# Optimization experiments

Measured on AMD Instinct MI355X. Metric: run time of the kernel, lower is better.

The kernel has to match this reference:

```python
import jax, jax.numpy as jnp
import numpy as np

B = 128      # graphs in batch
NPG = 128    # nodes per graph
F = 256      # num_node_features
D = 192      # d_model
NH = 8       # decoder heads
L = 4        # decoder layers
DFF = 512
DEG = 16     # avg degree
P = 32       # num_patch_nodes
EH = 96      # encoder_hidden = max(D//2, 48)
GH = 4       # GAT heads (layer 1)
EPS = 1e-5


def _init(key, shape, fan_in):
    return jax.random.normal(key, shape, jnp.float32) / np.sqrt(fan_in)


def setup_inputs() -> dict:
    key = jax.random.key(0)
    ks = jax.random.split(key, 40)
    N = B * NPG
    E = N * DEG
    off = jnp.repeat(jnp.arange(B, dtype=jnp.int32) * NPG, E // B)
    src = jax.random.randint(ks[1], (E,), 0, NPG, dtype=jnp.int32) + off
    dst = jax.random.randint(ks[2], (E,), 0, NPG, dtype=jnp.int32) + off
    inp = dict(
        subgraph_x=jax.random.normal(ks[0], (N, F), jnp.float32),
        subgraph_edge_index=jnp.stack([src, dst]),
        target_local_idx=jax.random.randint(ks[3], (B,), 0, NPG, dtype=jnp.int32),
        batch=jnp.repeat(jnp.arange(B, dtype=jnp.int32), NPG),
        num_patch_nodes=P,
    )
    # GAT encoder params (PyG GATConv layout: W [heads*out, in], att [heads, out])
    inp['gat1_w'] = _init(ks[4], (GH * EH, F), F)
    inp['gat1_att_src'] = _init(ks[5], (GH, EH), EH)
    inp['gat1_att_dst'] = _init(ks[6], (GH, EH), EH)
    inp['gat1_b'] = jnp.zeros((GH * EH,), jnp.float32)
    inp['gat2_w'] = _init(ks[7], (D, GH * EH), GH * EH)
    inp['gat2_att_src'] = _init(ks[8], (1, D), D)
    inp['gat2_att_dst'] = _init(ks[9], (1, D), D)
    inp['gat2_b'] = jnp.zeros((D,), jnp.float32)
    # TransformerDecoder layers (stacked over L)
    inp['sa_qkv_w'] = _init(ks[10], (L, 3 * D, D), D)
    inp['sa_qkv_b'] = jnp.zeros((L, 3 * D), jnp.float32)
    inp['sa_out_w'] = _init(ks[11], (L, D, D), D)
    inp['sa_out_b'] = jnp.zeros((L, D), jnp.float32)
    inp['ca_qkv_w'] = _init(ks[12], (L, 3 * D, D), D)
    inp['ca_qkv_b'] = jnp.zeros((L, 3 * D), jnp.float32)
    inp['ca_out_w'] = _init(ks[13], (L, D, D), D)
    inp['ca_out_b'] = jnp.zeros((L, D), jnp.float32)
    inp['ff1_w'] = _init(ks[14], (L, DFF, D), D)
    inp['ff1_b'] = jnp.zeros((L, DFF), jnp.float32)
    inp['ff2_w'] = _init(ks[15], (L, D, DFF), DFF)
    inp['ff2_b'] = jnp.zeros((L, D), jnp.float32)
    inp['ln_g'] = jnp.ones((L, 3, D), jnp.float32)
    inp['ln_b'] = jnp.zeros((L, 3, D), jnp.float32)
    # feature head
    inp['h1_w'] = _init(ks[16], (D, D), D)
    inp['h1_b'] = jnp.zeros((D,), jnp.float32)
    inp['h2_w'] = _init(ks[17], (F, D), D)
    inp['h2_b'] = jnp.zeros((F,), jnp.float32)
    return inp


def _gat(x, src, dst, W, a_src, a_dst, bias, heads, ch, concat):
    # PyG GATConv with add_self_loops=True, negative_slope=0.2, eval mode (no dropout)
    N = x.shape[0]
    xp = (x @ W.T).reshape(N, heads, ch)
    loop = jnp.arange(N, dtype=src.dtype)
    s = jnp.concatenate([src, loop])
    d = jnp.concatenate([dst, loop])
    al_s = (xp * a_src).sum(-1)  # [N, H]
    al_d = (xp * a_dst).sum(-1)
    e = jax.nn.leaky_relu(al_s[s] + al_d[d], 0.2)  # [E+N, H]
    emax = jax.ops.segment_max(e, d, num_segments=N)
    ex = jnp.exp(e - emax[d])
    den = jax.ops.segment_sum(ex, d, num_segments=N)
    coef = ex / (den[d] + 1e-16)
    out = jax.ops.segment_sum(xp[s] * coef[:, :, None], d, num_segments=N)  # [N,H,C]
    out = out.reshape(N, heads * ch) if concat else out.mean(1)
    return out + bias


def _ln(x, g, b):
    m = x.mean(-1, keepdims=True)
    v = ((x - m) ** 2).mean(-1, keepdims=True)
    return (x - m) / jnp.sqrt(v + EPS) * g + b


def _mha(q_in, kv_in, qkv_w, qkv_b, out_w, out_b, causal):
    b, sq, d = q_in.shape
    sk = kv_in.shape[1]
    dh = d // NH
    wq, wk, wv = jnp.split(qkv_w, 3, axis=0)
    bq, bk, bv = jnp.split(qkv_b, 3)
    q = (q_in @ wq.T + bq).reshape(b, sq, NH, dh).transpose(0, 2, 1, 3)
    k = (kv_in @ wk.T + bk).reshape(b, sk, NH, dh).transpose(0, 2, 1, 3)
    v = (kv_in @ wv.T + bv).reshape(b, sk, NH, dh).transpose(0, 2, 1, 3)
    sc = jnp.einsum('bhqd,bhkd->bhqk', q, k) / np.sqrt(dh).astype(np.float32)
    if causal:
        sc = jnp.where(jnp.tril(jnp.ones((sq, sk), bool)), sc, -1e30)
    a = jax.nn.softmax(sc, axis=-1)
    o = jnp.einsum('bhqk,bhkd->bhqd', a, v).transpose(0, 2, 1, 3).reshape(b, sq, d)
    return o @ out_w.T + out_b


def _pe(max_len, d):
    pos = jnp.arange(max_len, dtype=jnp.float32)[:, None]
    div = jnp.exp(jnp.arange(0, d, 2, dtype=jnp.float32) * (-np.log(10000.0) / d))
    pe = jnp.zeros((max_len, d), jnp.float32)
    return pe.at[:, 0::2].set(jnp.sin(pos * div)).at[:, 1::2].set(jnp.cos(pos * div))


def _forward(subgraph_x, gat1_w, gat1_att_src, gat1_att_dst, gat1_b,
             gat2_w, gat2_att_src, gat2_att_dst, gat2_b,
             sa_qkv_w, sa_qkv_b, sa_out_w, sa_out_b,
             ca_qkv_w, ca_qkv_b, ca_out_w, ca_out_b,
             ff1_w, ff1_b, ff2_w, ff2_b, ln_g, ln_b,
             h1_w, h1_b, h2_w, h2_b,
             subgraph_edge_index, target_local_idx, batch, num_patch_nodes):
    src, dst = subgraph_edge_index[0], subgraph_edge_index[1]
    h = jax.nn.elu(_gat(subgraph_x, src, dst, gat1_w, gat1_att_src, gat1_att_dst, gat1_b, GH, EH, True))
    mem = _gat(h, src, dst, gat2_w, gat2_att_src, gat2_att_dst, gat2_b, 1, D, False)
    bsz = target_local_idx.shape[0]
    mem_d = mem.reshape(bsz, -1, D)  # to_dense_batch: equal-sized, sorted graphs -> reshape, mask all-valid
    tgt = mem_d[jnp.arange(bsz), target_local_idx][:, None, :]  # [B,1,D]
    Pn = int(num_patch_nodes)
    pe = _pe(Pn + 1, D)
    feats = []
    adj = jnp.zeros((bsz, Pn + 1, Pn + 1), subgraph_x.dtype)
    for i in range(Pn):
        s = i + 1
        x = tgt + pe[None, :s]  # pos encoding (dropout is eval no-op)
        for l in range(L):
            x = _ln(x + _mha(x, x, sa_qkv_w[l], sa_qkv_b[l], sa_out_w[l], sa_out_b[l], True), ln_g[l, 0], ln_b[l, 0])
            x = _ln(x + _mha(x, mem_d, ca_qkv_w[l], ca_qkv_b[l], ca_out_w[l], ca_out_b[l], False), ln_g[l, 1], ln_b[l, 1])
            ff = jax.nn.gelu(x @ ff1_w[l].T + ff1_b[l], approximate=False) @ ff2_w[l].T + ff2_b[l]
            x = _ln(x + ff, ln_g[l, 2], ln_b[l, 2])
        last = x[:, -1]  # [B,D]
        feats.append(jax.nn.gelu(last @ h1_w.T + h1_b, approximate=False) @ h2_w.T + h2_b)
        cl = jnp.einsum('bsd,bd->bs', x, last)  # connection logits, len s
        adj = adj.at[:, i, Pn].set(cl[:, 0]).at[:, Pn, i].set(cl[:, 0])
        if i > 0:
            adj = adj.at[:, i, :i].set(cl[:, 1:i + 1]).at[:, :i, i].set(cl[:, 1:i + 1])
        tgt = jnp.concatenate([tgt, jax.lax.stop_gradient(last)[:, None]], axis=1)  # .detach() in torch
    adj = jnp.triu(adj, 1)
    adj = adj + jnp.swapaxes(adj, -1, -2)  # symmetric, zero diagonal
    return jnp.stack(feats, axis=1), adj


def reference(subgraph_x, subgraph_edge_index, target_local_idx, batch, num_patch_nodes,
              gat1_w, gat1_att_src, gat1_att_dst, gat1_b,
              gat2_w, gat2_att_src, gat2_att_dst, gat2_b,
              sa_qkv_w, sa_qkv_b, sa_out_w, sa_out_b,
              ca_qkv_w, ca_qkv_b, ca_out_w, ca_out_b,
              ff1_w, ff1_b, ff2_w, ff2_b, ln_g, ln_b,
              h1_w, h1_b, h2_w, h2_b):
    return _forward(subgraph_x, gat1_w, gat1_att_src, gat1_att_dst, gat1_b,
                    gat2_w, gat2_att_src, gat2_att_dst, gat2_b,
                    sa_qkv_w, sa_qkv_b, sa_out_w, sa_out_b,
                    ca_qkv_w, ca_qkv_b, ca_out_w, ca_out_b,
                    ff1_w, ff1_b, ff2_w, ff2_b, ln_g, ln_b,
                    h1_w, h1_b, h2_w, h2_b,
                    subgraph_edge_index, target_local_idx, batch, num_patch_nodes)
```

## Files before the change

kernel.cpp:

```cpp
#include <hip/hip_runtime.h>
#include <hip/hip_bf16.h>
#include <math.h>

#define DEV __device__ __forceinline__
typedef unsigned int u32;
typedef unsigned short u16;

constexpr int NNODES = 16384;
constexpr int NEDGE  = 262144;
constexpr int NEL    = NEDGE + NNODES;
constexpr int FIN    = 256;
constexpr int C1     = 384;
constexpr int DM     = 192;
constexpr int BZ     = 128;
constexpr int NPG_   = 128;
constexpr int LL     = 4;
constexpr int PP     = 32;
constexpr int SM     = 33;
constexpr int DFF_   = 512;

constexpr int PL4     = 52224;
constexpr int OFF4_QKV = 0;
constexpr int OFF4_SAO = 13824;
constexpr int OFF4_CAQ = 18432;
constexpr int OFF4_CAO = 23040;
constexpr int OFF4_FF1 = 27648;
constexpr int OFF4_FF2 = 39936;
constexpr int OFF4_H1  = 4*PL4;
constexpr int OFF4_H2  = OFF4_H1 + 4608;

constexpr size_t O_KVK = 0;
constexpr size_t O_VT  = 6291456;
constexpr size_t O_XP1 = 0;
constexpr size_t O_H   = 6291456;
constexpr size_t O_XP2 = 12582912;
constexpr size_t O_MEM = 15728640;
constexpr size_t O_VSAT= 18874368;
constexpr size_t O_WP  = 20545536;
constexpr size_t O_PE  = 21424128;
constexpr size_t O_AL1S= O_PE + 6336;
constexpr size_t O_AL1D= O_AL1S + 65536;
constexpr size_t O_AL2S= O_AL1D + 65536;
constexpr size_t O_AL2D= O_AL2S + 16384;
constexpr size_t O_CNT = O_AL2D + 16384;
constexpr size_t O_BASE= O_CNT + 16384;
constexpr size_t O_FILL= O_BASE + 16384;
constexpr size_t O_CSRC= O_FILL + 16384;

DEV float gelu_f(float v) { return 0.5f*v*(1.0f + erff(v*0.7071067811865475f)); }
DEV float bflo(u32 w) { return __uint_as_float(w << 16); }
DEV float bfhi(u32 w) { return __uint_as_float(w & 0xffff0000u); }
DEV float bfu(u16 u)  { return __uint_as_float(((u32)u) << 16); }
DEV u16 bf16u(float a) {
  __hip_bfloat16 h = __float2bfloat16(a);
  return *reinterpret_cast<u16*>(&h);
}
DEV u32 pk2(float a, float b) {
  return (u32)bf16u(a) | ((u32)bf16u(b) << 16);
}
DEV void fma8(float& a, uint4 w, float4 xa, float4 xb) {
  a = fmaf(bflo(w.x), xa.x, a); a = fmaf(bfhi(w.x), xa.y, a);
  a = fmaf(bflo(w.y), xa.z, a); a = fmaf(bfhi(w.y), xa.w, a);
  a = fmaf(bflo(w.z), xb.x, a); a = fmaf(bfhi(w.z), xb.y, a);
  a = fmaf(bflo(w.w), xb.z, a); a = fmaf(bfhi(w.w), xb.w, a);
}
template<int NU4, int STRIDE>
DEV float dotcol(const uint4* __restrict__ col, const float* __restrict__ xv) {
  const float4* x4 = (const float4*)xv;
  float a0 = 0, a1 = 0, a2 = 0, a3 = 0;
  #pragma unroll
  for (int q = 0; q < NU4; ++q) {
    uint4 w = col[(size_t)q*STRIDE];
    if ((q & 3) == 0) fma8(a0, w, x4[2*q], x4[2*q+1]);
    else if ((q & 3) == 1) fma8(a1, w, x4[2*q], x4[2*q+1]);
    else if ((q & 3) == 2) fma8(a2, w, x4[2*q], x4[2*q+1]);
    else fma8(a3, w, x4[2*q], x4[2*q+1]);
  }
  return (a0+a1)+(a2+a3);
}

__global__ void zero_kernel(float* adj, int* cnt, int* fill) {
  int i = blockIdx.x*256 + threadIdx.x;
  if (i < BZ*SM*SM) adj[i] = 0.f;
  if (i < NNODES) { cnt[i] = 0; fill[i] = 0; }
}

__global__ void pe_kernel(float* pe) {
  int idx = blockIdx.x*256 + threadIdx.x;
  if (idx >= SM*DM) return;
  int p = idx / DM, d = idx % DM;
  int i2 = d >> 1;
  float div = __expf((float)(2*i2) * (-9.210340371976184f / (float)DM));
  float a = (float)p * div;
  pe[idx] = (d & 1) ? cosf(a) : sinf(a);
}

__global__ void pack_kernel(const float* __restrict__ W, uint4* __restrict__ P, int N, int K) {
  int idx = blockIdx.x*256 + threadIdx.x;
  if (idx >= N*(K>>3)) return;
  int o = idx % N, kq = idx / N;
  const float* r = W + (size_t)o*K + 8*kq;
  uint4 u;
  u.x = pk2(r[0], r[1]); u.y = pk2(r[2], r[3]);
  u.z = pk2(r[4], r[5]); u.w = pk2(r[6], r[7]);
  P[idx] = u;
}

template<int BMODE, bool BF16OUT>
__global__ __launch_bounds__(256) void gemm_nt(const float* __restrict__ A,
    const float* __restrict__ W, const float* __restrict__ bias,
    float* __restrict__ Cf, __hip_bfloat16* __restrict__ Cb, int M, int N, int K)
{
  __shared__ float As[16][68];
  __shared__ float Ws[16][68];
  const int bm = blockIdx.y*64, bn = blockIdx.x*64;
  const int t = threadIdx.x, tx = t & 15, ty = t >> 4;
  float acc[4][4] = {};
  for (int k0 = 0; k0 < K; k0 += 16) {
    #pragma unroll
    for (int i = 0; i < 4; ++i) {
      int idx = t + i*256, kk = idx & 15, m = idx >> 4;
      As[kk][m] = A[(size_t)(bm+m)*K + k0+kk];
      Ws[kk][m] = W[(size_t)(bn+m)*K + k0+kk];
    }
    __syncthreads();
    #pragma unroll
    for (int kk = 0; kk < 16; ++kk) {
      const float4 a4 = *(const float4*)&As[kk][ty*4];
      const float4 b4 = *(const float4*)&Ws[kk][tx*4];
      const float av[4] = {a4.x,a4.y,a4.z,a4.w};
      const float bv[4] = {b4.x,b4.y,b4.z,b4.w};
      #pragma unroll
      for (int i = 0; i < 4; ++i)
        #pragma unroll
        for (int j = 0; j < 4; ++j)
          acc[i][j] = fmaf(av[i], bv[j], acc[i][j]);
    }
    __syncthreads();
  }
  #pragma unroll
  for (int i = 0; i < 4; ++i) {
    const int m = bm + ty*4 + i;
    #pragma unroll
    for (int j = 0; j < 4; ++j) {
      const int n = bn + tx*4 + j;
      float v = acc[i][j];
      if (BMODE == 1) v += bias[n];
      if (BMODE == 2) v += bias[m];
      if (BF16OUT) Cb[(size_t)m*N + n] = __float2bfloat16(v);
      else         Cf[(size_t)m*N + n] = v;
    }
  }
}

template<int HEADS, int CH>
__global__ void al_kernel(const float* __restrict__ xp, const float* __restrict__ asrc,
                          const float* __restrict__ adst, float* als, float* ald) {
  int idx = blockIdx.x*256 + threadIdx.x;
  if (idx >= NNODES*HEADS) return;
  int n = idx / HEADS, h = idx % HEADS;
  const float* row = xp + (size_t)n*(HEADS*CH) + h*CH;
  float s = 0, d = 0;
  for (int c = 0; c < CH; ++c) { float v = row[c]; s = fmaf(v, asrc[h*CH+c], s); d = fmaf(v, adst[h*CH+c], d); }
  als[idx] = s; ald[idx] = d;
}

__global__ void count_kernel(const int* __restrict__ dst, int* cnt) {
  int e = blockIdx.x*256 + threadIdx.x;
  if (e < NEDGE) atomicAdd(&cnt[dst[e]], 1);
}

__global__ __launch_bounds__(1024) void scan_kernel(const int* __restrict__ cnt, int* base) {
  __shared__ int tot[1024];
  int t = threadIdx.x;
  int local[16]; int s = 0;
  #pragma unroll
  for (int i = 0; i < 16; ++i) { int v = cnt[t*16+i] + 1; local[i] = s; s += v; }
  tot[t] = s; __syncthreads();
  if (t == 0) { int r = 0; for (int i = 0; i < 1024; ++i) { int v = tot[i]; tot[i] = r; r += v; } }
  __syncthreads();
  int off = tot[t];
  #pragma unroll
  for (int i = 0; i < 16; ++i) base[t*16+i] = off + local[i];
}

__global__ void scatter_kernel(const int* __restrict__ src, const int* __restrict__ dst,
                               const int* __restrict__ base, int* fill, int* csrc) {
  int e = blockIdx.x*256 + threadIdx.x;
  if (e < NEDGE) {
    int d = dst[e];
    int p = atomicAdd(&fill[d], 1);
    csrc[base[d] + p] = src[e];
  } else if (e < NEL) {
    int n = e - NEDGE;
    int p = atomicAdd(&fill[n], 1);
    csrc[base[n] + p] = n;
  }
}

template<int HEADS, int CH, bool ELU>
__global__ __launch_bounds__(128) void agg_kernel(const float* __restrict__ xp,
    const float* __restrict__ als, const float* __restrict__ ald,
    const int* __restrict__ cnt, const int* __restrict__ base, const int* __restrict__ csrc,
    const float* __restrict__ bias, float* __restrict__ out)
{
  constexpr int CO = HEADS*CH;
  constexpr int MAXD = 128;
  int n = blockIdx.x, t = threadIdx.x;
  int deg = cnt[n] + 1, st = base[n];
  if (deg > MAXD) deg = MAXD;
  __shared__ int   srcs[MAXD];
  __shared__ float ex[MAXD][HEADS];
  __shared__ float den[HEADS];
  for (int j = t; j < deg; j += 128) srcs[j] = csrc[st + j];
  __syncthreads();
  for (int idx = t; idx < deg*HEADS; idx += 128) {
    int j = idx / HEADS, h = idx % HEADS;
    float e = als[srcs[j]*HEADS + h] + ald[n*HEADS + h];
    ex[j][h] = (e > 0.f) ? e : 0.2f*e;
  }
  __syncthreads();
  if (t < HEADS) {
    float m = -1e30f;
    for (int j = 0; j < deg; ++j) m = fmaxf(m, ex[j][t]);
    float s = 0;
    for (int j = 0; j < deg; ++j) { float v = __expf(ex[j][t]-m); ex[j][t] = v; s += v; }
    den[t] = 1.0f/(s + 1e-16f);
  }
  __syncthreads();
  for (int c = t; c < CO; c += 128) {
    int h = c / CH;
    float acc = 0;
    for (int j = 0; j < deg; ++j) acc = fmaf(ex[j][h], xp[(size_t)srcs[j]*CO + c], acc);
    float v = acc*den[h] + bias[c];
    if (ELU) v = (v > 0.f) ? v : (__expf(v) - 1.0f);
    out[(size_t)n*CO + c] = v;
  }
}

__global__ __launch_bounds__(1024, 1) void decode_kernel(
    const float* __restrict__ mem, const u16* __restrict__ kvk, const u16* __restrict__ vT,
    const uint4* __restrict__ wp, const float* __restrict__ pe,
    u16* __restrict__ vsaT, const int* __restrict__ tgt_idx,
    const float* __restrict__ saqkvb, const float* __restrict__ saoutb,
    const float* __restrict__ caqkvb, const float* __restrict__ caoutb,
    const float* __restrict__ ff1b, const float* __restrict__ ff2b,
    const float* __restrict__ lng, const float* __restrict__ lnb,
    const float* __restrict__ h1b, const float* __restrict__ h2b,
    float* __restrict__ feats, float* __restrict__ adj)
{
  const int b = blockIdx.x, t = threadIdx.x;
  const int wv = t >> 6, lane = t & 63;
  __shared__ u16   ksa16[4*33*194];
  __shared__ float lasts[SM][193];
  __shared__ __align__(16) float x[DM];
  __shared__ __align__(16) float qkv[DM];
  __shared__ __align__(16) float attno[DM];
  __shared__ __align__(16) float hid[DFF_];
  __shared__ float prob[33*9 + 7];
  __shared__ float cprob[128*9 + 2];
  __shared__ __align__(16) float psA[1152];
  __shared__ float painv[8], cainv[8], red[16];
  const float scl = 0.2041241452319315f;
  const float* tgt0 = mem + ((size_t)b*NPG_ + tgt_idx[b])*DM;

  auto ln_ps4 = [&](const float* g, const float* be) {
    float v = 0.f;
    if (t < DM) v = x[t] + ((psA[t]+psA[192+t]) + (psA[384+t]+psA[576+t]));
    float s = v, q = v*v;
    #pragma unroll
    for (int o = 32; o; o >>= 1) { s += __shfl_down(s, o, 64); q += __shfl_down(q, o, 64); }
    if (lane == 0 && wv < 3) { red[wv] = s; red[8+wv] = q; }
    __syncthreads();
    float S = red[0]+red[1]+red[2];
    float Q = red[8]+red[9]+red[10];
    float mu = S*(1.f/DM), var = Q*(1.f/DM) - mu*mu;
    float rstd = rsqrtf(var + 1e-5f);
    if (t < DM) x[t] = (v-mu)*rstd*g[t] + be[t];
    __syncthreads();
  };
  auto skgemv4 = [&](const uint4* P, const float* xv, const float* bias) {
    if (t < 768) {
      int ks = t/192, o = t - ks*192;
      psA[t] = (ks ? 0.f : bias[o]) + dotcol<6,192>(P + ks*6*192 + o, xv + 48*ks);
    }
  };

  for (int i = 0; i < PP; ++i) {
    if (t < DM) x[t] = ((i == 0) ? tgt0[t] : lasts[i-1][t]) + pe[i*DM + t];
    __syncthreads();
    for (int l = 0; l < LL; ++l) {
      const uint4* WL = wp + (size_t)l*PL4;
      {
        int ks = t/576, o = t - ks*576;
        psA[t] = (ks ? 0.f : saqkvb[l*576+o]) + dotcol<12,576>(WL + OFF4_QKV + ks*12*576 + o, x + 96*ks);
        if (t < 128) {
          int o2 = 448 + t;
          psA[1024 + t] = dotcol<12,576>(WL + OFF4_QKV + 12*576 + o2, x + 96);
        }
      }
      __syncthreads();
      if (t < 576) {
        float a = psA[t] + psA[576+t];
        if (t < 192)      qkv[t] = a;
        else if (t < 384) ksa16[(l*33 + i)*194 + (t-192)] = bf16u(a);
        else              vsaT[((size_t)(b*4+l)*192 + (t-384))*34 + i] = bf16u(a);
      }
      __syncthreads();
      if (wv < 8) {
        float s = -1e30f;
        if (lane <= i) {
          const u32* kr = (const u32*)ksa16 + (l*33 + lane)*97 + wv*12;
          float a0 = 0, a1 = 0;
          #pragma unroll
          for (int c = 0; c < 12; c += 2) {
            u32 w0 = kr[c], w1 = kr[c+1];
            a0 = fmaf(bflo(w0), qkv[wv*24 + 2*c],   a0);
            a0 = fmaf(bfhi(w0), qkv[wv*24 + 2*c+1], a0);
            a1 = fmaf(bflo(w1), qkv[wv*24 + 2*c+2], a1);
            a1 = fmaf(bfhi(w1), qkv[wv*24 + 2*c+3], a1);
          }
          s = (a0+a1) * scl;
        }
        float m = s;
        #pragma unroll
        for (int o2 = 32; o2; o2 >>= 1) m = fmaxf(m, __shfl_xor(m, o2, 64));
        float e = (lane <= i) ? __expf(s - m) : 0.f;
        float sm = e;
        #pragma unroll
        for (int o2 = 32; o2; o2 >>= 1) sm += __shfl_xor(sm, o2, 64);
        if (lane <= i) prob[lane*9 + wv] = e;
        if (lane == 0) painv[wv] = 1.0f / sm;
      }
      __syncthreads();
      if (t < DM) {
        int hh = t / 24;
        const u16* vr = vsaT + ((size_t)(b*4+l)*192 + t)*34;
        float a0 = 0, a1 = 0;
        for (int j = 0; j + 1 <= i; j += 2) {
          a0 = fmaf(prob[j*9 + hh],     bfu(vr[j]),   a0);
          a1 = fmaf(prob[(j+1)*9 + hh], bfu(vr[j+1]), a1);
        }
        if (!(i & 1)) a0 = fmaf(prob[i*9 + hh], bfu(vr[i]), a0);
        attno[t] = (a0 + a1) * painv[hh];
      }
      __syncthreads();
      skgemv4(WL + OFF4_SAO, attno, saoutb + l*DM);
      __syncthreads();
      ln_ps4(lng + (l*3+0)*DM, lnb + (l*3+0)*DM);
      skgemv4(WL + OFF4_CAQ, x, caqkvb + l*3*DM);
      __syncthreads();
      if (t < DM) qkv[t] = (psA[t]+psA[192+t]) + (psA[384+t]+psA[576+t]);
      __syncthreads();
      {
        int j = t >> 3, hh = t & 7;
        const uint4* kr = (const uint4*)kvk + ((size_t)l*NNODES + b*NPG_ + j)*24 + hh*3;
        uint4 w0 = kr[0], w1 = kr[1], w2 = kr[2];
        const float4* q4 = (const float4*)qkv + hh*6;
        float a0 = 0, a1 = 0, a2 = 0;
        fma8(a0, w0, q4[0], q4[1]);
        fma8(a1, w1, q4[2], q4[3]);
        fma8(a2, w2, q4[4], q4[5]);
        cprob[j*9 + hh] = (a0+a1+a2) * scl;
      }
      __syncthreads();
      if (wv < 8) {
        float s0 = cprob[lane*9 + wv], s1 = cprob[(lane+64)*9 + wv];
        float m = fmaxf(s0, s1);
        #pragma unroll
        for (int o2 = 32; o2; o2 >>= 1) m = fmaxf(m, __shfl_xor(m, o2, 64));
        float e0 = __expf(s0-m), e1 = __expf(s1-m);
        float sm = e0+e1;
        #pragma unroll
        for (int o2 = 32; o2; o2 >>= 1) sm += __shfl_xor(sm, o2, 64);
        cprob[lane*9 + wv] = e0; cprob[(lane+64)*9 + wv] = e1;
        if (lane == 0) cainv[wv] = 1.0f / sm;
      }
      __syncthreads();
      if (t < 384) {
        int half = t/192, tm = t - half*192, hh = tm / 24;
        const uint4* v4 = (const uint4*)(vT + ((size_t)l*DM + tm)*NNODES + b*NPG_ + half*64);
        int jb = half*64;
        float a0 = 0, a1 = 0;
        #pragma unroll
        for (int q = 0; q < 8; ++q) {
          uint4 w = v4[q];
          int j0 = jb + q*8;
          a0 = fmaf(cprob[(j0+0)*9 + hh], bflo(w.x), a0);
          a1 = fmaf(cprob[(j0+1)*9 + hh], bfhi(w.x), a1);
          a0 = fmaf(cprob[(j0+2)*9 + hh], bflo(w.y), a0);
          a1 = fmaf(cprob[(j0+3)*9 + hh], bfhi(w.y), a1);
          a0 = fmaf(cprob[(j0+4)*9 + hh], bflo(w.z), a0);
          a1 = fmaf(cprob[(j0+5)*9 + hh], bfhi(w.z), a1);
          a0 = fmaf(cprob[(j0+6)*9 + hh], bflo(w.w), a0);
          a1 = fmaf(cprob[(j0+7)*9 + hh], bfhi(w.w), a1);
        }
        psA[half*192 + tm] = a0 + a1;
      }
      __syncthreads();
      if (t < DM) attno[t] = (psA[t] + psA[192+t]) * cainv[t/24];
      __syncthreads();
      skgemv4(WL + OFF4_CAO, attno, caoutb + l*DM);
      __syncthreads();
      ln_ps4(lng + (l*3+1)*DM, lnb + (l*3+1)*DM);
      {
        int ks = t >> 9, o = t & 511;
        psA[t] = (ks ? 0.f : ff1b[l*DFF_+o]) + dotcol<12,512>(WL + OFF4_FF1 + ks*12*512 + o, x + 96*ks);
      }
      __syncthreads();
      if (t < DFF_) hid[t] = gelu_f(psA[t] + psA[512+t]);
      __syncthreads();
      if (t < 768) {
        int ks = t/192, o = t - ks*192;
        psA[t] = (ks ? 0.f : ff2b[l*DM+o]) + dotcol<16,192>(WL + OFF4_FF2 + ks*16*192 + o, hid + 128*ks);
      }
      __syncthreads();
      ln_ps4(lng + (l*3+2)*DM, lnb + (l*3+2)*DM);
    }
    skgemv4(wp + OFF4_H1, x, h1b);
    __syncthreads();
    if (t < DM) {
      hid[t] = gelu_f((psA[t]+psA[192+t]) + (psA[384+t]+psA[576+t]));
      lasts[i][t] = x[t];
    }
    __syncthreads();
    {
      int ks = t >> 8, o = t & 255;
      psA[t] = (ks ? 0.f : h2b[o]) + dotcol<6,256>(wp + OFF4_H2 + ks*6*256 + o, hid + 48*ks);
    }
    __syncthreads();
    if (t < 256)
      feats[((size_t)b*PP + i)*256 + t] = (psA[t]+psA[256+t]) + (psA[512+t]+psA[768+t]);
    if (t <= i) {
      float a = 0.f;
      for (int d = 0; d < DM; ++d) a = fmaf(lasts[t][d], lasts[i][d], a);
      if (t == 0) {
        adj[((size_t)b*SM + i)*SM + 32] = a;
        adj[((size_t)b*SM + 32)*SM + i] = a;
      } else {
        int j2 = t - 1;
        adj[((size_t)b*SM + j2)*SM + i] = a;
        adj[((size_t)b*SM + i)*SM + j2] = a;
      }
    }
    __syncthreads();
  }
}

extern "C" void kernel_launch(void* const* d_in, const int* in_sizes, int n_in,
                              void* d_out, int out_size, void* d_ws, size_t ws_size,
                              hipStream_t stream) {
  (void)in_sizes; (void)n_in; (void)out_size; (void)ws_size;
  const float* x_in    = (const float*)d_in[0];
  const int*   ei      = (const int*)d_in[1];
  const int*   tgt_idx = (const int*)d_in[2];
  const float* gat1_w  = (const float*)d_in[5];
  const float* g1as    = (const float*)d_in[6];
  const float* g1ad    = (const float*)d_in[7];
  const float* g1b     = (const float*)d_in[8];
  const float* gat2_w  = (const float*)d_in[9];
  const float* g2as    = (const float*)d_in[10];
  const float* g2ad    = (const float*)d_in[11];
  const float* g2b     = (const float*)d_in[12];
  const float* saqkvw  = (const float*)d_in[13];
  const float* saqkvb  = (const float*)d_in[14];
  const float* saoutw  = (const float*)d_in[15];
  const float* saoutb  = (const float*)d_in[16];
  const float* caqkvw  = (const float*)d_in[17];
  const float* caqkvb  = (const float*)d_in[18];
  const float* caoutw  = (const float*)d_in[19];
  const float* caoutb  = (const float*)d_in[20];
  const float* ff1w    = (const float*)d_in[21];
  const float* ff1b    = (const float*)d_in[22];
  const float* ff2w    = (const float*)d_in[23];
  const float* ff2b    = (const float*)d_in[24];
  const float* lng     = (const float*)d_in[25];
  const float* lnb     = (const float*)d_in[26];
  const float* h1w     = (const float*)d_in[27];
  const float* h1b     = (const float*)d_in[28];
  const float* h2w     = (const float*)d_in[29];
  const float* h2b     = (const float*)d_in[30];

  float* ws  = (float*)d_ws;
  float* out = (float*)d_out;
  float* adj = out + (size_t)BZ*PP*256;

  const int* src = ei;
  const int* dst = ei + NEDGE;

  int* cnt  = (int*)(ws + O_CNT);
  int* base = (int*)(ws + O_BASE);
  int* fill = (int*)(ws + O_FILL);
  int* csrc = (int*)(ws + O_CSRC);

  hipLaunchKernelGGL(zero_kernel, dim3(545), dim3(256), 0, stream, adj, cnt, fill);

  hipLaunchKernelGGL((gemm_nt<0,false>), dim3(C1/64, NNODES/64), dim3(256), 0, stream,
                     x_in, gat1_w, (const float*)nullptr, ws + O_XP1, (__hip_bfloat16*)nullptr,
                     NNODES, C1, FIN);
  hipLaunchKernelGGL((al_kernel<4,96>), dim3(NNODES*4/256), dim3(256), 0, stream,
                     ws+O_XP1, g1as, g1ad, ws+O_AL1S, ws+O_AL1D);
  hipLaunchKernelGGL(count_kernel, dim3(NEDGE/256), dim3(256), 0, stream, dst, cnt);
  hipLaunchKernelGGL(scan_kernel, dim3(1), dim3(1024), 0, stream, cnt, base);
  hipLaunchKernelGGL(scatter_kernel, dim3(NEL/256), dim3(256), 0, stream, src, dst, base, fill, csrc);
  hipLaunchKernelGGL((agg_kernel<4,96,true>), dim3(NNODES), dim3(128), 0, stream,
                     ws+O_XP1, ws+O_AL1S, ws+O_AL1D, cnt, base, csrc, g1b, ws+O_H);

  hipLaunchKernelGGL((gemm_nt<0,false>), dim3(DM/64, NNODES/64), dim3(256), 0, stream,
                     ws+O_H, gat2_w, (const float*)nullptr, ws+O_XP2, (__hip_bfloat16*)nullptr,
                     NNODES, DM, C1);
  hipLaunchKernelGGL((al_kernel<1,192>), dim3(NNODES/256), dim3(256), 0, stream,
                     ws+O_XP2, g2as, g2ad, ws+O_AL2S, ws+O_AL2D);
  hipLaunchKernelGGL((agg_kernel<1,192,false>), dim3(NNODES), dim3(128), 0, stream,
                     ws+O_XP2, ws+O_AL2S, ws+O_AL2D, cnt, base, csrc, g2b, ws+O_MEM);

  uint4* wp = (uint4*)(ws + O_WP);
  auto PK = [&](const float* Wsrc, int off_u4, int N, int K) {
    hipLaunchKernelGGL(pack_kernel, dim3((N*(K/8)+255)/256), dim3(256), 0, stream,
                       Wsrc, wp + off_u4, N, K);
  };
  for (int l = 0; l < LL; ++l) {
    PK(saqkvw + (size_t)l*110592, l*PL4 + OFF4_QKV, 576, 192);
    PK(saoutw + (size_t)l*36864,  l*PL4 + OFF4_SAO, 192, 192);
    PK(caqkvw + (size_t)l*110592, l*PL4 + OFF4_CAQ, 192, 192);
    PK(caoutw + (size_t)l*36864,  l*PL4 + OFF4_CAO, 192, 192);
    PK(ff1w   + (size_t)l*98304,  l*PL4 + OFF4_FF1, 512, 192);
    PK(ff2w   + (size_t)l*98304,  l*PL4 + OFF4_FF2, 192, 512);
  }
  PK(h1w, OFF4_H1, 192, 192);
  PK(h2w, OFF4_H2, 256, 192);

  hipLaunchKernelGGL(pe_kernel, dim3((SM*DM+255)/256), dim3(256), 0, stream, ws+O_PE);

  __hip_bfloat16* kvk = (__hip_bfloat16*)(ws + O_KVK);
  __hip_bfloat16* vT  = (__hip_bfloat16*)(ws + O_VT);
  for (int l = 0; l < LL; ++l) {
    hipLaunchKernelGGL((gemm_nt<1,true>), dim3(DM/64, NNODES/64), dim3(256), 0, stream,
                       ws+O_MEM, caqkvw + (size_t)l*110592 + (size_t)192*192,
                       caqkvb + l*576 + 192, (float*)nullptr,
                       kvk + (size_t)l*NNODES*DM, NNODES, DM, DM);
    hipLaunchKernelGGL((gemm_nt<2,true>), dim3(NNODES/64, DM/64), dim3(256), 0, stream,
                       caqkvw + (size_t)l*110592 + (size_t)2*192*192, ws+O_MEM,
                       caqkvb + l*576 + 384, (float*)nullptr,
                       vT + (size_t)l*DM*NNODES, DM, NNODES, DM);
  }

  hipLaunchKernelGGL(decode_kernel, dim3(BZ), dim3(1024), 0, stream,
                     ws+O_MEM, (const u16*)kvk, (const u16*)vT, wp, ws+O_PE,
                     (u16*)(ws+O_VSAT), tgt_idx,
                     saqkvb, saoutb, caqkvb, caoutb, ff1b, ff2b, lng, lnb, h1b, h2b,
                     out, adj);
}
```

Measured before the change: 4.499 ms.

## Prefetch decoder weights into registers ahead of use and keep self-attn V in LDS

The decode kernel now issues the global loads for each next GEMV's weight columns into register buffers one stage early. A custom barrier waits only on LDS counters, so those global loads stay in flight across barriers. Self-attention V values move from a global scratch buffer into shared memory, and the cross-attention value pass is folded into a single 192-thread loop. The next step's input setup is merged into the tail stage, which removes a barrier. The goal is to hide global weight-load latency in this latency-bound serial decode loop. The cost is heavy register pressure at 1024 threads per block, with a possible spill around the final layer, where several prefetch buffers overlap.

```diff
diff --git a/kernel.cpp b/kernel.cpp
--- a/kernel.cpp
+++ b/kernel.cpp
@@ -35,7 +35,6 @@
 constexpr size_t O_H   = 6291456;
 constexpr size_t O_XP2 = 12582912;
 constexpr size_t O_MEM = 15728640;
-constexpr size_t O_VSAT= 18874368;
 constexpr size_t O_WP  = 20545536;
 constexpr size_t O_PE  = 21424128;
 constexpr size_t O_AL1S= O_PE + 6336;
@@ -75,6 +74,26 @@
     else if ((q & 3) == 1) fma8(a1, w, x4[2*q], x4[2*q+1]);
     else if ((q & 3) == 2) fma8(a2, w, x4[2*q], x4[2*q+1]);
     else fma8(a3, w, x4[2*q], x4[2*q+1]);
+  }
+  return (a0+a1)+(a2+a3);
+}
+template<int N> struct WB { uint4 w[N]; };
+template<int N, int STRIDE>
+DEV void wissue(WB<N>& r, const uint4* __restrict__ col) {
+  #pragma unroll
+  for (int q = 0; q < N; ++q) r.w[q] = col[(size_t)q*STRIDE];
+}
+template<int N>
+DEV float wuse(const WB<N>& r, const float* __restrict__ xv) {
+  const float4* x4 = (const float4*)xv;
+  float a0 = 0, a1 = 0, a2 = 0, a3 = 0;
+  #pragma unroll
+  for (int q = 0; q < N; ++q) {
+    float4 xa = x4[2*q], xb = x4[2*q+1];
+    if ((q & 3) == 0) fma8(a0, r.w[q], xa, xb);
+    else if ((q & 3) == 1) fma8(a1, r.w[q], xa, xb);
+    else if ((q & 3) == 2) fma8(a2, r.w[q], xa, xb);
+    else fma8(a3, r.w[q], xa, xb);
   }
   return (a0+a1)+(a2+a3);
 }
@@ -241,7 +260,7 @@
 __global__ __launch_bounds__(1024, 1) void decode_kernel(
     const float* __restrict__ mem, const u16* __restrict__ kvk, const u16* __restrict__ vT,
     const uint4* __restrict__ wp, const float* __restrict__ pe,
-    u16* __restrict__ vsaT, const int* __restrict__ tgt_idx,
+    const int* __restrict__ tgt_idx,
     const float* __restrict__ saqkvb, const float* __restrict__ saoutb,
     const float* __restrict__ caqkvb, const float* __restrict__ caoutb,
     const float* __restrict__ ff1b, const float* __restrict__ ff2b,
@@ -252,6 +271,7 @@
   const int b = blockIdx.x, t = threadIdx.x;
   const int wv = t >> 6, lane = t & 63;
   __shared__ u16   ksa16[4*33*194];
+  __shared__ u16   vsa16[4*33*194];
   __shared__ float lasts[SM][193];
   __shared__ __align__(16) float x[DM];
   __shared__ __align__(16) float qkv[DM];
@@ -263,6 +283,18 @@
   __shared__ float painv[8], cainv[8], red[16];
   const float scl = 0.2041241452319315f;
   const float* tgt0 = mem + ((size_t)b*NPG_ + tgt_idx[b])*DM;
+  const uint4* kvk4 = (const uint4*)kvk;
+
+  const int qks = t / 576, qcol = t - qks*576;
+  const int k4s = t >> 9,  o512 = t & 511;
+  const int ks4 = (t < 768) ? t/192 : 0;
+  const int o192 = t - ((t < 768) ? (t/192)*192 : 0);
+  const int ks2h = t >> 8, o256 = t & 255;
+  const int caj = t >> 3, cah = t & 7;
+
+  WB<12> rQKV; WB<3> rCAK; WB<6> rSAO, rCAQ, rCAO, rH1, rH2; WB<12> rFF1; WB<16> rFF2;
+
+  auto barL = [&]() { asm volatile("s_waitcnt lgkmcnt(0)\n\ts_barrier" ::: "memory"); };
 
   auto ln_ps4 = [&](const float* g, const float* be) {
     float v = 0.f;
@@ -271,46 +303,42 @@
     #pragma unroll
     for (int o = 32; o; o >>= 1) { s += __shfl_down(s, o, 64); q += __shfl_down(q, o, 64); }
     if (lane == 0 && wv < 3) { red[wv] = s; red[8+wv] = q; }
-    __syncthreads();
+    barL();
     float S = red[0]+red[1]+red[2];
     float Q = red[8]+red[9]+red[10];
     float mu = S*(1.f/DM), var = Q*(1.f/DM) - mu*mu;
     float rstd = rsqrtf(var + 1e-5f);
     if (t < DM) x[t] = (v-mu)*rstd*g[t] + be[t];
-    __syncthreads();
+    barL();
   };
-  auto skgemv4 = [&](const uint4* P, const float* xv, const float* bias) {
-    if (t < 768) {
-      int ks = t/192, o = t - ks*192;
-      psA[t] = (ks ? 0.f : bias[o]) + dotcol<6,192>(P + ks*6*192 + o, xv + 48*ks);
-    }
-  };
+
+  if (t < DM) x[t] = tgt0[t] + pe[t];
+  wissue<12,576>(rQKV, wp + OFF4_QKV + qks*12*576 + qcol);
+  barL();
 
   for (int i = 0; i < PP; ++i) {
-    if (t < DM) x[t] = ((i == 0) ? tgt0[t] : lasts[i-1][t]) + pe[i*DM + t];
-    __syncthreads();
     for (int l = 0; l < LL; ++l) {
       const uint4* WL = wp + (size_t)l*PL4;
       {
-        int ks = t/576, o = t - ks*576;
-        psA[t] = (ks ? 0.f : saqkvb[l*576+o]) + dotcol<12,576>(WL + OFF4_QKV + ks*12*576 + o, x + 96*ks);
-        if (t < 128) {
-          int o2 = 448 + t;
-          psA[1024 + t] = dotcol<12,576>(WL + OFF4_QKV + 12*576 + o2, x + 96);
-        }
-      }
-      __syncthreads();
+        psA[t] = (qks ? 0.f : saqkvb[l*576 + qcol]) + wuse<12>(rQKV, x + 96*qks);
+        if (t < 128)
+          psA[1024 + t] = dotcol<12,576>(WL + OFF4_QKV + 12*576 + 448 + t, x + 96);
+      }
+      wissue<3,1>(rCAK, kvk4 + ((size_t)l*NNODES + b*NPG_ + caj)*24 + cah*3);
+      barL();
       if (t < 576) {
-        float a = psA[t] + psA[576+t];
+        float sec = (t < 448) ? psA[576 + t] : psA[1024 + (t - 448)];
+        float a = psA[t] + sec;
         if (t < 192)      qkv[t] = a;
         else if (t < 384) ksa16[(l*33 + i)*194 + (t-192)] = bf16u(a);
-        else              vsaT[((size_t)(b*4+l)*192 + (t-384))*34 + i] = bf16u(a);
-      }
-      __syncthreads();
+        else              vsa16[(l*33 + i)*194 + (t-384)] = bf16u(a);
+      }
+      if (t < 768) wissue<6,192>(rSAO, WL + OFF4_SAO + ks4*6*192 + o192);
+      barL();
       if (wv < 8) {
         float s = -1e30f;
         if (lane <= i) {
-          const u32* kr = (const u32*)ksa16 + (l*33 + lane)*97 + wv*12;
+          const u32* kr = (const u32*)ksa16 + ((size_t)l*33 + lane)*97 + wv*12;
           float a0 = 0, a1 = 0;
           #pragma unroll
           for (int c = 0; c < 12; c += 2) {
@@ -332,38 +360,34 @@
         if (lane <= i) prob[lane*9 + wv] = e;
         if (lane == 0) painv[wv] = 1.0f / sm;
       }
-      __syncthreads();
+      barL();
       if (t < DM) {
         int hh = t / 24;
-        const u16* vr = vsaT + ((size_t)(b*4+l)*192 + t)*34;
+        const u16* vr = vsa16 + (size_t)l*33*194 + t;
         float a0 = 0, a1 = 0;
         for (int j = 0; j + 1 <= i; j += 2) {
-          a0 = fmaf(prob[j*9 + hh],     bfu(vr[j]),   a0);
-          a1 = fmaf(prob[(j+1)*9 + hh], bfu(vr[j+1]), a1);
+          a0 = fmaf(prob[j*9 + hh],     bfu(vr[(size_t)j*194]),     a0);
+          a1 = fmaf(prob[(j+1)*9 + hh], bfu(vr[(size_t)(j+1)*194]), a1);
         }
-        if (!(i & 1)) a0 = fmaf(prob[i*9 + hh], bfu(vr[i]), a0);
+        if (!(i & 1)) a0 = fmaf(prob[i*9 + hh], bfu(vr[(size_t)i*194]), a0);
         attno[t] = (a0 + a1) * painv[hh];
       }
-      __syncthreads();
-      skgemv4(WL + OFF4_SAO, attno, saoutb + l*DM);
-      __syncthreads();
+      barL();
+      if (t < 768) {
+        psA[t] = (ks4 ? 0.f : saoutb[l*DM + o192]) + wuse<6>(rSAO, attno + 48*ks4);
+        wissue<6,192>(rCAQ, WL + OFF4_CAQ + ks4*6*192 + o192);
+      }
+      barL();
       ln_ps4(lng + (l*3+0)*DM, lnb + (l*3+0)*DM);
-      skgemv4(WL + OFF4_CAQ, x, caqkvb + l*3*DM);
-      __syncthreads();
+      if (t < 768) {
+        psA[t] = (ks4 ? 0.f : caqkvb[l*3*DM + o192]) + wuse<6>(rCAQ, x + 48*ks4);
+        wissue<6,192>(rCAO, WL + OFF4_CAO + ks4*6*192 + o192);
+      }
+      barL();
       if (t < DM) qkv[t] = (psA[t]+psA[192+t]) + (psA[384+t]+psA[576+t]);
-      __syncthreads();
-      {
-        int j = t >> 3, hh = t & 7;
-        const uint4* kr = (const uint4*)kvk + ((size_t)l*NNODES + b*NPG_ + j)*24 + hh*3;
-        uint4 w0 = kr[0], w1 = kr[1], w2 = kr[2];
-        const float4* q4 = (const float4*)qkv + hh*6;
-        float a0 = 0, a1 = 0, a2 = 0;
-        fma8(a0, w0, q4[0], q4[1]);
-        fma8(a1, w1, q4[2], q4[3]);
-        fma8(a2, w2, q4[4], q4[5]);
-        cprob[j*9 + hh] = (a0+a1+a2) * scl;
-      }
-      __syncthreads();
+      barL();
+      cprob[caj*9 + cah] = scl * wuse<3>(rCAK, qkv + cah*24);
+      barL();
       if (wv < 8) {
         float s0 = cprob[lane*9 + wv], s1 = cprob[(lane+64)*9 + wv];
         float m = fmaxf(s0, s1);
@@ -376,16 +400,15 @@
         cprob[lane*9 + wv] = e0; cprob[(lane+64)*9 + wv] = e1;
         if (lane == 0) cainv[wv] = 1.0f / sm;
       }
-      __syncthreads();
-      if (t < 384) {
-        int half = t/192, tm = t - half*192, hh = tm / 24;
-        const uint4* v4 = (const uint4*)(vT + ((size_t)l*DM + tm)*NNODES + b*NPG_ + half*64);
-        int jb = half*64;
+      barL();
+      if (t < DM) {
+        int hh = t / 24;
+        const uint4* v4 = (const uint4*)(vT + ((size_t)l*DM + t)*NNODES + b*NPG_);
         float a0 = 0, a1 = 0;
         #pragma unroll
-        for (int q = 0; q < 8; ++q) {
+        for (int q = 0; q < 16; ++q) {
           uint4 w = v4[q];
-          int j0 = jb + q*8;
+          int j0 = q*8;
           a0 = fmaf(cprob[(j0+0)*9 + hh], bflo(w.x), a0);
           a1 = fmaf(cprob[(j0+1)*9 + hh], bfhi(w.x), a1);
           a0 = fmaf(cprob[(j0+2)*9 + hh], bflo(w.y), a0);
@@ -395,55 +418,56 @@
           a0 = fmaf(cprob[(j0+6)*9 + hh], bflo(w.w), a0);
           a1 = fmaf(cprob[(j0+7)*9 + hh], bfhi(w.w), a1);
         }
-        psA[half*192 + tm] = a0 + a1;
-      }
-      __syncthreads();
-      if (t < DM) attno[t] = (psA[t] + psA[192+t]) * cainv[t/24];
-      __syncthreads();
-      skgemv4(WL + OFF4_CAO, attno, caoutb + l*DM);
-      __syncthreads();
+        attno[t] = (a0 + a1) * cainv[hh];
+      }
+      barL();
+      if (t < 768) psA[t] = (ks4 ? 0.f : caoutb[l*DM + o192]) + wuse<6>(rCAO, attno + 48*ks4);
+      wissue<12,512>(rFF1, WL + OFF4_FF1 + k4s*12*512 + o512);
+      barL();
       ln_ps4(lng + (l*3+1)*DM, lnb + (l*3+1)*DM);
-      {
-        int ks = t >> 9, o = t & 511;
-        psA[t] = (ks ? 0.f : ff1b[l*DFF_+o]) + dotcol<12,512>(WL + OFF4_FF1 + ks*12*512 + o, x + 96*ks);
-      }
-      __syncthreads();
+      psA[t] = (k4s ? 0.f : ff1b[l*DFF_ + o512]) + wuse<12>(rFF1, x + 96*k4s);
+      if (t < 768) wissue<16,192>(rFF2, WL + OFF4_FF2 + ks4*16*192 + o192);
+      barL();
       if (t < DFF_) hid[t] = gelu_f(psA[t] + psA[512+t]);
-      __syncthreads();
-      if (t < 768) {
-        int ks = t/192, o = t - ks*192;
-        psA[t] = (ks ? 0.f : ff2b[l*DM+o]) + dotcol<16,192>(WL + OFF4_FF2 + ks*16*192 + o, hid + 128*ks);
-      }
-      __syncthreads();
+      barL();
+      if (t < 768) psA[t] = (ks4 ? 0.f : ff2b[l*DM + o192]) + wuse<16>(rFF2, hid + 128*ks4);
+      if (l < 3) {
+        wissue<12,576>(rQKV, wp + (size_t)(l+1)*PL4 + OFF4_QKV + qks*12*576 + qcol);
+      } else {
+        if (t < 768) wissue<6,192>(rH1, wp + OFF4_H1 + ks4*6*192 + o192);
+        wissue<6,256>(rH2, wp + OFF4_H2 + ks2h*6*256 + o256);
+        wissue<12,576>(rQKV, wp + OFF4_QKV + qks*12*576 + qcol);
+      }
+      barL();
       ln_ps4(lng + (l*3+2)*DM, lnb + (l*3+2)*DM);
     }
-    skgemv4(wp + OFF4_H1, x, h1b);
-    __syncthreads();
+    if (t < 768) psA[t] = (ks4 ? 0.f : h1b[o192]) + wuse<6>(rH1, x + 48*ks4);
+    barL();
     if (t < DM) {
       hid[t] = gelu_f((psA[t]+psA[192+t]) + (psA[384+t]+psA[576+t]));
       lasts[i][t] = x[t];
     }
-    __syncthreads();
-    {
-      int ks = t >> 8, o = t & 255;
-      psA[t] = (ks ? 0.f : h2b[o]) + dotcol<6,256>(wp + OFF4_H2 + ks*6*256 + o, hid + 48*ks);
-    }
-    __syncthreads();
-    if (t < 256)
+    barL();
+    psA[t] = (ks2h ? 0.f : h2b[o256]) + wuse<6>(rH2, hid + 48*ks2h);
+    barL();
+    if (t < 256) {
       feats[((size_t)b*PP + i)*256 + t] = (psA[t]+psA[256+t]) + (psA[512+t]+psA[768+t]);
-    if (t <= i) {
+    } else if (t < 289 && (t - 256) <= i) {
+      int jj = t - 256;
       float a = 0.f;
-      for (int d = 0; d < DM; ++d) a = fmaf(lasts[t][d], lasts[i][d], a);
-      if (t == 0) {
+      for (int d = 0; d < DM; ++d) a = fmaf(lasts[jj][d], lasts[i][d], a);
+      if (jj == 0) {
         adj[((size_t)b*SM + i)*SM + 32] = a;
         adj[((size_t)b*SM + 32)*SM + i] = a;
       } else {
-        int j2 = t - 1;
-        adj[((size_t)b*SM + j2)*SM + i] = a;
-        adj[((size_t)b*SM + i)*SM + j2] = a;
-      }
+        adj[((size_t)b*SM + jj-1)*SM + i] = a;
+        adj[((size_t)b*SM + i)*SM + jj-1] = a;
+      }
+    } else if (t >= 512 && t < 704) {
+      int d = t - 512;
+      x[d] = lasts[i][d] + pe[(i+1)*DM + d];
     }
-    __syncthreads();
+    barL();
   }
 }
 
@@ -546,8 +570,7 @@
   }
 
   hipLaunchKernelGGL(decode_kernel, dim3(BZ), dim3(1024), 0, stream,
-                     ws+O_MEM, (const u16*)kvk, (const u16*)vT, wp, ws+O_PE,
-                     (u16*)(ws+O_VSAT), tgt_idx,
+                     ws+O_MEM, (const u16*)kvk, (const u16*)vT, wp, ws+O_PE, tgt_idx,
                      saqkvb, saoutb, caqkvb, caoutb, ff1b, ff2b, lng, lnb, h1b, h2b,
                      out, adj);
 }
```

Result: slower. 11.61 ms (+158.0%).
